# Kernel optimization log

Hardware: AMD Instinct MI355X
Metric: run time of the kernel (lower is better)

Reference implementation:

```python
import jax, jax.numpy as jnp
import numpy as np

ALG_DIM = 248      # dim of E8 adjoint rep
NNZ_BASE = 300     # base structure-constant triples (antisymmetrized -> 600 nnz)
N_NODES = 20000
N_EDGES = 160000


def _structure_constants():
    """Deterministic sparse antisymmetric structure constants C_ijk.

    Returns index arrays (ci, cj, ck) int32 and values cv float32 such that
    [x, y]_k = sum_t cv[t] * x[ci[t]] * y[cj[t]] with C antisymmetric in (i, j).
    """
    rng = np.random.default_rng(0)
    i = rng.integers(0, ALG_DIM, NNZ_BASE)
    j = rng.integers(0, ALG_DIM, NNZ_BASE)
    j = np.where(j == i, (j + 1) % ALG_DIM, j)  # bracket of equal basis elts is 0
    k = rng.integers(0, ALG_DIM, NNZ_BASE)
    v = rng.normal(size=NNZ_BASE).astype(np.float32)
    ci = np.concatenate([i, j]).astype(np.int32)
    cj = np.concatenate([j, i]).astype(np.int32)
    ck = np.concatenate([k, k]).astype(np.int32)
    cv = np.concatenate([v, -v]).astype(np.float32)
    return jnp.asarray(ci), jnp.asarray(cj), jnp.asarray(ck), jnp.asarray(cv)


def _bracket(x, y, ci, cj, ck, cv):
    """Sparse Lie bracket [x, y]: x, y have shape (..., ALG_DIM)."""
    terms = x[..., ci] * y[..., cj] * cv          # (..., nnz)
    return jnp.zeros(x.shape, x.dtype).at[..., ck].add(terms)


def setup_inputs() -> dict:
    key = jax.random.key(0)
    k1, k2 = jax.random.split(key)
    features = jax.random.normal(k1, (N_NODES, ALG_DIM), dtype=jnp.float32)
    edge_index = jax.random.randint(k2, (2, N_EDGES), 0, N_NODES, dtype=jnp.int32)
    ci, cj, ck, cv = _structure_constants()
    return {
        "features": features,
        "edge_index": edge_index,
        "ci": ci, "cj": cj, "ck": ck, "cv": cv,
        "alpha_msg": jnp.float32(1.0),     # msg_projection.alpha
        "alpha_bil": jnp.float32(1.0),     # msg_bilinear.alpha
        "alpha_w": jnp.float32(1.0),       # update_W.alpha
        "update_scale": jnp.float32(0.1),
    }


def reference(features, edge_index, ci, cj, ck, cv,
              alpha_msg, alpha_bil, alpha_w, update_scale):
    src_idx = edge_index[0]
    tgt_idx = edge_index[1]
    src = features[src_idx]                        # (E, d) gather
    tgt = features[tgt_idx]                        # (E, d) gather
    # message: alpha_bil * [alpha_msg * src, tgt]
    msg = alpha_bil * _bracket(alpha_msg * src, tgt, ci, cj, ck, cv)
    # scatter-add aggregate into per-node accumulator
    agg = jnp.zeros_like(features).at[tgt_idx].add(msg)
    # bracket-based update: x + agg + scale * [agg, alpha_w * agg]
    upd = _bracket(agg, alpha_w * agg, ci, cj, ck, cv)
    return features + agg + update_scale * upd
```

## Files before the change

### kernel.cpp

```cpp
#include <hip/hip_runtime.h>
#include <hip/hip_fp16.h>


#define ALG    248
#define ALG4    62
#define SLOTS   32
#define WPB      2
#define TPB    128
#define MAXSL    8

struct __align__(8) Term { unsigned ijk; float v; };

__global__ __launch_bounds__(256) void elc_fill(
    const int* __restrict__ ei, int E,
    int* __restrict__ cnt, int* __restrict__ slot,
    const int* __restrict__ ci, const int* __restrict__ cj,
    const int* __restrict__ ck, const float* __restrict__ cv,
    Term* __restrict__ terms, int nnzB,
    const float* __restrict__ feat, uint2* __restrict__ feat16, int N)
{
    const int gt = blockIdx.x * 256 + threadIdx.x;
    const int gs = gridDim.x * 256;

    for (int e = gt; e < E; e += gs) {
        const int t = ei[E + e];
        const int p = atomicAdd(&cnt[t], 1);
        if (p < SLOTS) slot[t * SLOTS + p] = ei[e];
    }
    for (int t = gt; t < MAXSL * 64; t += gs) {
        Term tm; tm.ijk = 0u; tm.v = 0.f;
        if (t < nnzB) {
            tm.ijk = (unsigned)ci[t] | ((unsigned)cj[t] << 8)
                   | ((unsigned)ck[t] << 16);
            tm.v = cv[t];
        }
        terms[t] = tm;
    }
    if (feat16) {
        const int M = N * ALG4;
        const float4* f4 = (const float4*)feat;
        for (int i = gt; i < M; i += gs) {
            const float4 v = f4[i];
            const __half2 lo = __float22half2_rn(make_float2(v.x, v.y));
            const __half2 hi = __float22half2_rn(make_float2(v.z, v.w));
            uint2 o;
            o.x = *(const unsigned*)&lo;
            o.y = *(const unsigned*)&hi;
            feat16[i] = o;
        }
    }
}

__global__ __launch_bounds__(TPB, 8) void elc_node16(
    const float* __restrict__ feat,
    const uint2* __restrict__ feat16,
    const int*   __restrict__ cnt,
    const int*   __restrict__ slot,
    const Term*  __restrict__ terms,
    const float* __restrict__ p_am, const float* __restrict__ p_ab,
    float* __restrict__ out, int N, int nnzB)
{
    __shared__ __align__(16) float s_buf[WPB][512];
    __shared__ __align__(16) float s_ag[WPB][256];

    const int tid  = threadIdx.x;
    const int lane = tid & 63;
    const int wave = tid >> 6;

    int nSl = (nnzB + 63) >> 6;
    if (nSl > MAXSL) nSl = MAXSL;

    const int n = blockIdx.x * WPB + wave;
    if (n >= N) return;

    const int deg = min(cnt[n], SLOTS);
    const int sn  = slot[n * SLOTS + (lane & (SLOTS - 1))];
    const float4* feat4 = (const float4*)feat;
    float4 tgt = make_float4(0.f, 0.f, 0.f, 0.f);
    if (lane < ALG4) tgt = feat4[(size_t)n * ALG4 + lane];

    unsigned tijk[MAXSL];
    float    tval[MAXSL];
#pragma unroll
    for (int sl = 0; sl < MAXSL; ++sl) { tijk[sl] = 0u; tval[sl] = 0.f; }
    for (int sl = 0; sl < nSl; ++sl) {
        const Term tm = terms[(sl << 6) + lane];
        tijk[sl] = tm.ijk; tval[sl] = tm.v;
    }

    uint2 h[12];
#pragma unroll
    for (int d = 0; d < 12; ++d) {
        h[d] = make_uint2(0u, 0u);
        const int sd = __shfl(sn, d);
        if (d < deg && lane < ALG4)
            h[d] = feat16[(size_t)sd * ALG4 + lane];
    }
    __builtin_amdgcn_sched_barrier(0);

    float4 acc = make_float4(0.f, 0.f, 0.f, 0.f);
#pragma unroll
    for (int d = 0; d < 12; ++d) {
        const float2 lo = __half22float2(*(const __half2*)&h[d].x);
        const float2 hi = __half22float2(*(const __half2*)&h[d].y);
        acc.x += lo.x; acc.y += lo.y; acc.z += hi.x; acc.w += hi.y;
    }
    for (int d = 12; d < deg; ++d) {
        const int sd = __shfl(sn, d);
        if (lane < ALG4) {
            const uint2 hd = feat16[(size_t)sd * ALG4 + lane];
            const float2 lo = __half22float2(*(const __half2*)&hd.x);
            const float2 hi = __half22float2(*(const __half2*)&hd.y);
            acc.x += lo.x; acc.y += lo.y; acc.z += hi.x; acc.w += hi.y;
        }
    }

    const float cab = (*p_ab) * (*p_am);
    float* sbuf = s_buf[wave];
    float* ag   = s_ag[wave];

    if (lane < ALG4) {
        ((float4*)sbuf)[2 * lane]     = make_float4(acc.x, tgt.x, acc.y, tgt.y);
        ((float4*)sbuf)[2 * lane + 1] = make_float4(acc.z, tgt.z, acc.w, tgt.w);
    }
    ((float4*)ag)[lane] = make_float4(0.f, 0.f, 0.f, 0.f);

    auto doSlot = [&](int sl) {
        const unsigned p = tijk[sl];
        const int i2 = (int)((p & 255u) << 1);
        const int j2 = (int)(((p >> 8) & 255u) << 1);
        const float2 a = *(const float2*)(sbuf + i2);
        const float2 b = *(const float2*)(sbuf + j2);
        float d = a.x * b.y;
        d = fmaf(-b.x, a.y, d);
        atomicAdd(ag + (int)((p >> 16) & 255u), tval[sl] * d);
    };
    if (nSl == 5) {
#pragma unroll
        for (int sl = 0; sl < 5; ++sl) doSlot(sl);
    } else {
        for (int sl = 0; sl < nSl; ++sl) doSlot(sl);
    }

    if (lane < ALG4) {
        const float4 av = ((const float4*)ag)[lane];
        float4 o;
        o.x = fmaf(cab, av.x, tgt.x);
        o.y = fmaf(cab, av.y, tgt.y);
        o.z = fmaf(cab, av.z, tgt.z);
        o.w = fmaf(cab, av.w, tgt.w);
        ((float4*)(out + (size_t)n * ALG))[lane] = o;
    }
}

__global__ __launch_bounds__(TPB, 5) void elc_node32(
    const float* __restrict__ feat,
    const int*   __restrict__ cnt,
    const int*   __restrict__ slot,
    const Term*  __restrict__ terms,
    const float* __restrict__ p_am, const float* __restrict__ p_ab,
    float* __restrict__ out, int N, int nnzB)
{
    __shared__ __align__(16) float s_buf[WPB][512];
    __shared__ __align__(16) float s_ag[WPB][256];

    const int tid  = threadIdx.x;
    const int lane = tid & 63;
    const int wave = tid >> 6;

    int nSl = (nnzB + 63) >> 6;
    if (nSl > MAXSL) nSl = MAXSL;

    const int n = blockIdx.x * WPB + wave;
    if (n >= N) return;

    const int deg = min(cnt[n], SLOTS);
    const int sn  = slot[n * SLOTS + (lane & (SLOTS - 1))];
    const float4* feat4 = (const float4*)feat;
    float4 tgt = make_float4(0.f, 0.f, 0.f, 0.f);
    if (lane < ALG4) tgt = feat4[(size_t)n * ALG4 + lane];

    unsigned tijk[MAXSL];
    float    tval[MAXSL];
#pragma unroll
    for (int sl = 0; sl < MAXSL; ++sl) { tijk[sl] = 0u; tval[sl] = 0.f; }
    for (int sl = 0; sl < nSl; ++sl) {
        const Term tm = terms[(sl << 6) + lane];
        tijk[sl] = tm.ijk; tval[sl] = tm.v;
    }

    float4 acc = make_float4(0.f, 0.f, 0.f, 0.f);
    for (int d = 0; d < deg; ++d) {
        const int sd = __shfl(sn, d);
        if (lane < ALG4) {
            const float4 fd = feat4[(size_t)sd * ALG4 + lane];
            acc.x += fd.x; acc.y += fd.y; acc.z += fd.z; acc.w += fd.w;
        }
    }

    const float cab = (*p_ab) * (*p_am);
    float* sbuf = s_buf[wave];
    float* ag   = s_ag[wave];

    if (lane < ALG4) {
        ((float4*)sbuf)[2 * lane]     = make_float4(acc.x, tgt.x, acc.y, tgt.y);
        ((float4*)sbuf)[2 * lane + 1] = make_float4(acc.z, tgt.z, acc.w, tgt.w);
    }
    ((float4*)ag)[lane] = make_float4(0.f, 0.f, 0.f, 0.f);

    for (int sl = 0; sl < nSl; ++sl) {
        const unsigned p = tijk[sl];
        const int i2 = (int)((p & 255u) << 1);
        const int j2 = (int)(((p >> 8) & 255u) << 1);
        const float2 a = *(const float2*)(sbuf + i2);
        const float2 b = *(const float2*)(sbuf + j2);
        float d = a.x * b.y;
        d = fmaf(-b.x, a.y, d);
        atomicAdd(ag + (int)((p >> 16) & 255u), tval[sl] * d);
    }

    if (lane < ALG4) {
        const float4 av = ((const float4*)ag)[lane];
        float4 o;
        o.x = fmaf(cab, av.x, tgt.x);
        o.y = fmaf(cab, av.y, tgt.y);
        o.z = fmaf(cab, av.z, tgt.z);
        o.w = fmaf(cab, av.w, tgt.w);
        ((float4*)(out + (size_t)n * ALG))[lane] = o;
    }
}

extern "C" void kernel_launch(void* const* d_in, const int* in_sizes, int n_in,
                              void* d_out, int out_size, void* d_ws, size_t ws_size,
                              hipStream_t stream) {
    const float* feat = (const float*)d_in[0];
    const int*   ei   = (const int*)d_in[1];
    const int*   ci   = (const int*)d_in[2];
    const int*   cj   = (const int*)d_in[3];
    const int*   ck   = (const int*)d_in[4];
    const float* cv   = (const float*)d_in[5];
    const float* p_am = (const float*)d_in[6];
    const float* p_ab = (const float*)d_in[7];
    float* out = (float*)d_out;

    const int N    = in_sizes[0] / ALG;
    const int E    = in_sizes[1] / 2;
    const int nnz  = in_sizes[5];
    const int nnzB = nnz >> 1;

    char* w = (char*)d_ws;
    int*  cnt   = (int*)w;               w += ((size_t)N * 4 + 255) & ~255ull;
    int*  slot  = (int*)w;               w += ((size_t)N * SLOTS * 4 + 255) & ~255ull;
    Term* terms = (Term*)w;              w += ((size_t)MAXSL * 64 * 8 + 255) & ~255ull;
    uint2* feat16 = (uint2*)w;           w += (size_t)N * ALG4 * 8;
    const bool use16 = ((size_t)(w - (char*)d_ws) <= ws_size);

    hipMemsetAsync(cnt, 0, (size_t)N * sizeof(int), stream);
    elc_fill<<<1024, 256, 0, stream>>>(ei, E, cnt, slot, ci, cj, ck, cv,
                                       terms, nnzB, feat,
                                       use16 ? feat16 : (uint2*)nullptr, N);

    const int nblk = (N + WPB - 1) / WPB;
    if (use16)
        elc_node16<<<nblk, TPB, 0, stream>>>(feat, feat16, cnt, slot, terms,
                                             p_am, p_ab, out, N, nnzB);
    else
        elc_node32<<<nblk, TPB, 0, stream>>>(feat, cnt, slot, terms,
                                             p_am, p_ab, out, N, nnzB);
}
```

Baseline: 142.8 us.

## Derive node degree from sentinel-filled slots and load target row in fp16

The count and slot arrays are merged and memset to -1, so the node kernel can get each node's degree from a ballot over valid slot entries instead of a separate count read. The fp16 path now reads the target row from the half-precision copy rather than the fp32 features, and neighbours 12-19 are fetched as a second batched prefetch. Launch bounds and the fill grid size are also retuned. In exchange the memset covers the whole slot array, which is much larger, and the passthrough feature term loses precision by going through fp16.

```diff
diff --git a/kernel.cpp b/kernel.cpp
--- a/kernel.cpp
+++ b/kernel.cpp
@@ -24,8 +24,8 @@
 
     for (int e = gt; e < E; e += gs) {
         const int t = ei[E + e];
-        const int p = atomicAdd(&cnt[t], 1);
-        if (p < SLOTS) slot[t * SLOTS + p] = ei[e];
+        const int q = atomicAdd(&cnt[t], 1) + 1;
+        if (q >= 0 && q < SLOTS) slot[t * SLOTS + q] = ei[e];
     }
     for (int t = gt; t < MAXSL * 64; t += gs) {
         Term tm; tm.ijk = 0u; tm.v = 0.f;
@@ -51,10 +51,8 @@
     }
 }
 
-__global__ __launch_bounds__(TPB, 8) void elc_node16(
-    const float* __restrict__ feat,
+__global__ __launch_bounds__(TPB, 6) void elc_node16(
     const uint2* __restrict__ feat16,
-    const int*   __restrict__ cnt,
     const int*   __restrict__ slot,
     const Term*  __restrict__ terms,
     const float* __restrict__ p_am, const float* __restrict__ p_ab,
@@ -73,11 +71,10 @@
     const int n = blockIdx.x * WPB + wave;
     if (n >= N) return;
 
-    const int deg = min(cnt[n], SLOTS);
-    const int sn  = slot[n * SLOTS + (lane & (SLOTS - 1))];
-    const float4* feat4 = (const float4*)feat;
-    float4 tgt = make_float4(0.f, 0.f, 0.f, 0.f);
-    if (lane < ALG4) tgt = feat4[(size_t)n * ALG4 + lane];
+    const int sn = slot[n * SLOTS + (lane & (SLOTS - 1))];
+
+    uint2 th = make_uint2(0u, 0u);
+    if (lane < ALG4) th = feat16[(size_t)n * ALG4 + lane];
 
     unsigned tijk[MAXSL];
     float    tval[MAXSL];
@@ -88,13 +85,27 @@
         tijk[sl] = tm.ijk; tval[sl] = tm.v;
     }
 
+    const unsigned long long vm =
+        __ballot(lane < SLOTS && sn >= 0);
+    const int deg = __popcll(vm);
+
+    int sds[12];
+#pragma unroll
+    for (int d = 0; d < 12; ++d) sds[d] = __shfl(sn, d);
+
+    float4 tgt;
+    {
+        const float2 lo = __half22float2(*(const __half2*)&th.x);
+        const float2 hi = __half22float2(*(const __half2*)&th.y);
+        tgt = make_float4(lo.x, lo.y, hi.x, hi.y);
+    }
+
     uint2 h[12];
 #pragma unroll
     for (int d = 0; d < 12; ++d) {
         h[d] = make_uint2(0u, 0u);
-        const int sd = __shfl(sn, d);
         if (d < deg && lane < ALG4)
-            h[d] = feat16[(size_t)sd * ALG4 + lane];
+            h[d] = feat16[(size_t)sds[d] * ALG4 + lane];
     }
     __builtin_amdgcn_sched_barrier(0);
 
@@ -105,13 +116,31 @@
         const float2 hi = __half22float2(*(const __half2*)&h[d].y);
         acc.x += lo.x; acc.y += lo.y; acc.z += hi.x; acc.w += hi.y;
     }
-    for (int d = 12; d < deg; ++d) {
-        const int sd = __shfl(sn, d);
-        if (lane < ALG4) {
-            const uint2 hd = feat16[(size_t)sd * ALG4 + lane];
-            const float2 lo = __half22float2(*(const __half2*)&hd.x);
-            const float2 hi = __half22float2(*(const __half2*)&hd.y);
+
+    if (deg > 12) {
+        uint2 g[8];
+#pragma unroll
+        for (int d = 0; d < 8; ++d) {
+            g[d] = make_uint2(0u, 0u);
+            const int sd = __shfl(sn, d + 12);
+            if (d + 12 < deg && lane < ALG4)
+                g[d] = feat16[(size_t)sd * ALG4 + lane];
+        }
+        __builtin_amdgcn_sched_barrier(0);
+#pragma unroll
+        for (int d = 0; d < 8; ++d) {
+            const float2 lo = __half22float2(*(const __half2*)&g[d].x);
+            const float2 hi = __half22float2(*(const __half2*)&g[d].y);
             acc.x += lo.x; acc.y += lo.y; acc.z += hi.x; acc.w += hi.y;
+        }
+        for (int d = 20; d < deg; ++d) {
+            const int sd = __shfl(sn, d);
+            if (lane < ALG4) {
+                const uint2 hd = feat16[(size_t)sd * ALG4 + lane];
+                const float2 lo = __half22float2(*(const __half2*)&hd.x);
+                const float2 hi = __half22float2(*(const __half2*)&hd.y);
+                acc.x += lo.x; acc.y += lo.y; acc.z += hi.x; acc.w += hi.y;
+            }
         }
     }
 
@@ -155,7 +184,6 @@
 
 __global__ __launch_bounds__(TPB, 5) void elc_node32(
     const float* __restrict__ feat,
-    const int*   __restrict__ cnt,
     const int*   __restrict__ slot,
     const Term*  __restrict__ terms,
     const float* __restrict__ p_am, const float* __restrict__ p_ab,
@@ -174,8 +202,10 @@
     const int n = blockIdx.x * WPB + wave;
     if (n >= N) return;
 
-    const int deg = min(cnt[n], SLOTS);
-    const int sn  = slot[n * SLOTS + (lane & (SLOTS - 1))];
+    const int sn = slot[n * SLOTS + (lane & (SLOTS - 1))];
+    const unsigned long long vm = __ballot(lane < SLOTS && sn >= 0);
+    const int deg = __popcll(vm);
+
     const float4* feat4 = (const float4*)feat;
     float4 tgt = make_float4(0.f, 0.f, 0.f, 0.f);
     if (lane < ALG4) tgt = feat4[(size_t)n * ALG4 + lane];
@@ -249,22 +279,23 @@
     const int nnzB = nnz >> 1;
 
     char* w = (char*)d_ws;
-    int*  cnt   = (int*)w;               w += ((size_t)N * 4 + 255) & ~255ull;
-    int*  slot  = (int*)w;               w += ((size_t)N * SLOTS * 4 + 255) & ~255ull;
+    int*  cnt   = (int*)w;
+    int*  slot  = cnt + N;
+    w += ((size_t)N * (1 + SLOTS) * 4 + 255) & ~255ull;
     Term* terms = (Term*)w;              w += ((size_t)MAXSL * 64 * 8 + 255) & ~255ull;
     uint2* feat16 = (uint2*)w;           w += (size_t)N * ALG4 * 8;
     const bool use16 = ((size_t)(w - (char*)d_ws) <= ws_size);
 
-    hipMemsetAsync(cnt, 0, (size_t)N * sizeof(int), stream);
-    elc_fill<<<1024, 256, 0, stream>>>(ei, E, cnt, slot, ci, cj, ck, cv,
+    hipMemsetAsync(cnt, 0xFF, (size_t)N * (1 + SLOTS) * sizeof(int), stream);
+    elc_fill<<<2048, 256, 0, stream>>>(ei, E, cnt, slot, ci, cj, ck, cv,
                                        terms, nnzB, feat,
                                        use16 ? feat16 : (uint2*)nullptr, N);
 
     const int nblk = (N + WPB - 1) / WPB;
     if (use16)
-        elc_node16<<<nblk, TPB, 0, stream>>>(feat, feat16, cnt, slot, terms,
+        elc_node16<<<nblk, TPB, 0, stream>>>(feat16, slot, terms,
                                              p_am, p_ab, out, N, nnzB);
     else
-        elc_node32<<<nblk, TPB, 0, stream>>>(feat, cnt, slot, terms,
+        elc_node32<<<nblk, TPB, 0, stream>>>(feat, slot, terms,
                                              p_am, p_ab, out, N, nnzB);
 }
```

Result: no change. 141.4 us (-1.0%).
